# Kernel optimization log

Measured on AMD Instinct MI355X. Metric: run time of the kernel, lower is better.

The kernel has to match this reference:

```python
import jax, jax.numpy as jnp
import numpy as np
from jax import lax

N, CIN, H, W = 32, 128, 64, 64
COUT, KH, KW = 256, 3, 3
STRIDE = (1, 1)
PADDING = ((1, 1), (1, 1))


def setup_inputs() -> dict:
    key = jax.random.key(0)
    k1, k2, k3, k4 = jax.random.split(key, 4)
    # binary input in {0,1}
    x = jax.random.randint(k1, (N, CIN, H, W), 0, 2).astype(jnp.float32)
    # ternary weight in {-1,0,1}
    weight = (jax.random.randint(k2, (COUT, CIN, KH, KW), 0, 3) - 1).astype(jnp.float32)
    # integer bias (folded from BN, floored to int per get_sign_bias_from_bn)
    bias = jax.random.randint(k3, (COUT,), -200, 200).astype(jnp.float32)
    # sign in {-1,+1}, broadcast shape (1, COUT, 1, 1)
    sign = jnp.where(jax.random.bernoulli(k4, 0.5, (1, COUT, 1, 1)), 1.0, -1.0).astype(jnp.float32)
    return {"x": x, "weight": weight, "bias": bias, "sign": sign}


def reference(x, weight, bias, sign):
    # y = conv2d(x, W) + bias  (stride 1, pad 1, NCHW)
    y = lax.conv_general_dilated(
        x, weight,
        window_strides=STRIDE,
        padding=PADDING,
        dimension_numbers=("NCHW", "OIHW", "NCHW"),
    ) + bias[None, :, None, None]
    # rounding=True -> torch.round_(y)
    y = jnp.round(y)
    # output = 1 iff sign * y >= 0, cast back to input dtype
    return jnp.where(y * sign >= 0, jnp.float32(1), jnp.float32(0)).astype(x.dtype)
```

## Files before the change

kernel.cpp:

```cpp
#include <hip/hip_runtime.h>
#include <cstdint>


#define NIMG 32
#define CIN  128
#define HH   64
#define WW   64
#define COUT 256
#define PH   66
#define XT_ROWSTRIDE (PH * CIN)
#define XT_NSTRIDE   (PH * PH * CIN)
#define XT_BYTES     ((size_t)NIMG * XT_NSTRIDE)
#define WP_TAPSTRIDE (COUT * CIN)
#define WP_BYTES     ((size_t)9 * WP_TAPSTRIDE)

typedef int   v4i  __attribute__((ext_vector_type(4)));
typedef int   v16i __attribute__((ext_vector_type(16)));

__global__ __launch_bounds__(256) void xt_prepass(const float* __restrict__ x,
                                                  int8_t* __restrict__ xt) {
    const int py = blockIdx.x;
    const int n  = blockIdx.y;
    const int t  = threadIdx.x;
    int8_t* rowbase = xt + (size_t)(n * PH + py) * XT_ROWSTRIDE;

    if (py == 0 || py == PH - 1) {
        int4 z = {0, 0, 0, 0};
        for (int j = t; j < XT_ROWSTRIDE / 16; j += 256)
            ((int4*)rowbase)[j] = z;
        return;
    }

    __shared__ __align__(16) int8_t Ls[64 * 144];
    const int y  = py - 1;
    const int xq = t & 15;
    const float4* xf = (const float4*)x;
#pragma unroll
    for (int j = 0; j < 8; ++j) {
        const int ci = (t >> 4) + j * 16;
        float4 v = xf[((size_t)(n * CIN + ci) * HH + y) * 16 + xq];
        const int xv = xq * 4;
        Ls[(xv + 0) * 144 + ci] = (int8_t)v.x;
        Ls[(xv + 1) * 144 + ci] = (int8_t)v.y;
        Ls[(xv + 2) * 144 + ci] = (int8_t)v.z;
        Ls[(xv + 3) * 144 + ci] = (int8_t)v.w;
    }
    __syncthreads();
    const int4 z = {0, 0, 0, 0};
    for (int j = t; j < XT_ROWSTRIDE / 16; j += 256) {
        const int px  = j >> 3;
        const int c   = j & 7;
        int4 val;
        if (px == 0 || px == PH - 1) val = z;
        else                         val = *(const int4*)&Ls[(px - 1) * 144 + c * 16];
        *(int4*)(rowbase + (size_t)px * CIN + ((c ^ (px & 7)) << 4)) = val;
    }
}

__global__ __launch_bounds__(256) void w_prepack(const float* __restrict__ w,
                                                 int8_t* __restrict__ wq) {
    const int idx = blockIdx.x * 256 + threadIdx.x;
    if (idx >= (int)WP_BYTES) return;
    const int tap = idx >> 15;
    const int rem = idx & 32767;
    const int co  = rem >> 7;
    const int ci  = rem & 127;
    const int s = ci >> 5, hi = (ci >> 4) & 1, b = ci & 15;
    const int co32 = co >> 5, lo = co & 31;
    wq[(((tap * 8 + co32) * 4 + s) << 10) + ((hi * 32 + lo) << 4) + b] =
        (int8_t)w[(size_t)(co * CIN + ci) * 9 + tap];
}

__device__ __forceinline__ void glds16(const void* g, uint32_t lds_off) {
    asm volatile("s_mov_b32 m0, %0\n"
                 "global_load_lds_dwordx4 %1, off"
                 :: "s"(lds_off), "v"(g) : "memory");
}

__global__ __launch_bounds__(256) void binconv_gemm(
    const int8_t* __restrict__ xt, const int8_t* __restrict__ wq,
    const float* __restrict__ bias, const float* __restrict__ sign,
    float* __restrict__ out) {

    __shared__ __align__(16) int8_t Xraw[4 * XT_ROWSTRIDE];

    const int t    = threadIdx.x;
    const int wid  = t >> 6;
    const int lane = t & 63;
    const int bx   = blockIdx.x;
    const int co0  = blockIdx.y * 128;
    const int n    = bx >> 5;
    const int y0   = (bx & 31) << 1;

    const int8_t* xbase = xt + (size_t)n * XT_NSTRIDE + (size_t)y0 * XT_ROWSTRIDE;
    {
        const int8_t* gsrc = xbase + lane * 16;
        const uint32_t lds0 = (uint32_t)(uintptr_t)Xraw;
        for (int j = wid; j < 33; j += 4)
            glds16(gsrc + j * 1024,
                   __builtin_amdgcn_readfirstlane(lds0 + j * 1024));
        asm volatile("s_waitcnt vmcnt(0)" ::: "memory");
        __syncthreads();
    }

    const int m_lo = lane & 31;
    const int hi   = lane >> 5;
    const int co_off = (wid >> 1) * 64;
    const int yw     = wid & 1;
    const int ct0  = (co0 + co_off) >> 5;

    const int8_t* Xw  = Xraw + yw * XT_ROWSTRIDE;
    const int8_t* wqb = wq + lane * 16;

    v16i acc[2][2] = {};

#pragma unroll
    for (int tap = 0; tap < 9; ++tap) {
        const int ky = tap / 3, kx = tap % 3;
        const int8_t* xl = Xw + ky * XT_ROWSTRIDE;
        const int px0 = m_lo + kx;
        const int pk  = px0 & 7;

        v4i af[2][4];
#pragma unroll
        for (int c = 0; c < 2; ++c)
#pragma unroll
            for (int s = 0; s < 4; ++s)
                af[c][s] = *(const v4i*)(wqb
                    + ((((tap * 8 + ct0 + c) * 4) + s) << 10));

        const int8_t* xb = xl + px0 * CIN;
        v4i bf[2][4];
#pragma unroll
        for (int s = 0; s < 4; ++s) {
            const int sw = ((2 * s + hi) ^ pk) << 4;
#pragma unroll
            for (int m = 0; m < 2; ++m)
                bf[m][s] = *(const v4i*)(xb + m * 32 * CIN + sw);
        }
#pragma unroll
        for (int s = 0; s < 4; ++s)
#pragma unroll
            for (int c = 0; c < 2; ++c)
#pragma unroll
                for (int m = 0; m < 2; ++m)
                    acc[c][m] = __builtin_amdgcn_mfma_i32_32x32x32_i8(
                        af[c][s], bf[m][s], acc[c][m], 0, 0, 0);
    }

    const float* bco = bias + co0 + co_off;
    const float* sco = sign + co0 + co_off;
    float* outb = out + ((size_t)n * COUT + co0 + co_off) * (HH * WW)
                + (y0 + yw) * WW;
#pragma unroll
    for (int c = 0; c < 2; ++c) {
#pragma unroll
        for (int r = 0; r < 16; ++r) {
            const int co_l = c * 32 + (r & 3) + 8 * (r >> 2) + 4 * hi;
            const int bi = (int)bco[co_l];
            const int si = (int)sco[co_l];
            float* orow = outb + (size_t)co_l * (HH * WW);
#pragma unroll
            for (int m = 0; m < 2; ++m) {
                const int tv = (acc[c][m][r] + bi) * si;
                orow[m * 32 + m_lo] = (tv >= 0) ? 1.0f : 0.0f;
            }
        }
    }
}

__global__ __launch_bounds__(256) void naive_conv(
    const float* __restrict__ x, const float* __restrict__ w,
    const float* __restrict__ bias, const float* __restrict__ sign,
    float* __restrict__ out) {
    const int idx = blockIdx.x * 256 + threadIdx.x;
    const int xc = idx & 63, y = (idx >> 6) & 63, co = (idx >> 12) & 255,
              n = idx >> 20;
    float s = 0.f;
    for (int ci = 0; ci < CIN; ++ci)
        for (int ky = 0; ky < 3; ++ky) {
            const int iy = y + ky - 1;
            if (iy < 0 || iy >= HH) continue;
            for (int kx = 0; kx < 3; ++kx) {
                const int ix = xc + kx - 1;
                if (ix < 0 || ix >= WW) continue;
                s += x[((size_t)(n * CIN + ci) * HH + iy) * WW + ix] *
                     w[((size_t)(co * CIN + ci) * 3 + ky) * 3 + kx];
            }
        }
    const float yv = s + bias[co];
    out[idx] = ((sign[co] > 0.f) ? (yv >= 0.f) : (yv <= 0.f)) ? 1.0f : 0.0f;
}

extern "C" void kernel_launch(void* const* d_in, const int* in_sizes, int n_in,
                              void* d_out, int out_size, void* d_ws, size_t ws_size,
                              hipStream_t stream) {
    const float* x    = (const float*)d_in[0];
    const float* w    = (const float*)d_in[1];
    const float* bias = (const float*)d_in[2];
    const float* sign = (const float*)d_in[3];
    float* out = (float*)d_out;

    const size_t need = XT_BYTES + WP_BYTES;
    if (ws_size < need) {
        naive_conv<<<dim3((NIMG * COUT * HH * WW) / 256), 256, 0, stream>>>(
            x, w, bias, sign, out);
        return;
    }
    int8_t* xt = (int8_t*)d_ws;
    int8_t* wq = (int8_t*)d_ws + XT_BYTES;

    xt_prepass<<<dim3(PH, NIMG), 256, 0, stream>>>(x, xt);
    w_prepack<<<dim3((int)(WP_BYTES + 255) / 256), 256, 0, stream>>>(w, wq);
    binconv_gemm<<<dim3(NIMG * (HH / 2), COUT / 128), 256, 0, stream>>>(
        xt, wq, bias, sign, out);
}
```

Baseline: 228.3 us.

## Switch binary conv GEMM to FP4 scaled MFMA with LDS-staged vectorized output

Activations and ternary weights are now packed into 4-bit FP4 (E2M1) codes, two per byte. The GEMM uses the scaled f8f6f4 MFMA (32x32x64) with unit scales in place of int8 32x32x32, which halves the K steps and the bytes staged into LDS. The epilogue writes thresholded bits to LDS first, then emits coalesced 16-byte nontemporal float4 stores instead of scattered scalar stores. The price is bit-packing work in the prepass and reliance on FP4 encoding being exact for values in {-1,0,1}, plus fp32 accumulation staying exact for integer sums.

```diff
diff --git a/kernel.cpp b/kernel.cpp
--- a/kernel.cpp
+++ b/kernel.cpp
@@ -8,25 +8,32 @@
 #define WW   64
 #define COUT 256
 #define PH   66
-#define XT_ROWSTRIDE (PH * CIN)
-#define XT_NSTRIDE   (PH * PH * CIN)
-#define XT_BYTES     ((size_t)NIMG * XT_NSTRIDE)
-#define WP_TAPSTRIDE (COUT * CIN)
-#define WP_BYTES     ((size_t)9 * WP_TAPSTRIDE)
+#define X4_ROW 4224
+#define X4_IMG (PH * X4_ROW)
+#define X4_BYTES ((size_t)NIMG * X4_IMG)
+#define WQ4_BYTES ((size_t)9 * 8 * 2 * 64 * 16)
 
 typedef int   v4i  __attribute__((ext_vector_type(4)));
-typedef int   v16i __attribute__((ext_vector_type(16)));
+typedef int   v8i  __attribute__((ext_vector_type(8)));
+typedef float v16f __attribute__((ext_vector_type(16)));
+typedef float v4f  __attribute__((ext_vector_type(4)));
+
+__device__ __forceinline__ uint32_t pack4(uint32_t u) {
+    const uint32_t tt = (u & 0x01010101u) << 1;
+    return (tt & 0xFu) | ((tt >> 4) & 0xF0u) | ((tt >> 8) & 0xF00u)
+         | ((tt >> 12) & 0xF000u);
+}
 
 __global__ __launch_bounds__(256) void xt_prepass(const float* __restrict__ x,
-                                                  int8_t* __restrict__ xt) {
+                                                  int8_t* __restrict__ xt4) {
     const int py = blockIdx.x;
     const int n  = blockIdx.y;
     const int t  = threadIdx.x;
-    int8_t* rowbase = xt + (size_t)(n * PH + py) * XT_ROWSTRIDE;
+    int8_t* rowbase = xt4 + (size_t)(n * PH + py) * X4_ROW;
 
     if (py == 0 || py == PH - 1) {
         int4 z = {0, 0, 0, 0};
-        for (int j = t; j < XT_ROWSTRIDE / 16; j += 256)
+        for (int j = t; j < X4_ROW / 16; j += 256)
             ((int4*)rowbase)[j] = z;
         return;
     }
@@ -46,29 +53,38 @@
         Ls[(xv + 3) * 144 + ci] = (int8_t)v.w;
     }
     __syncthreads();
-    const int4 z = {0, 0, 0, 0};
-    for (int j = t; j < XT_ROWSTRIDE / 16; j += 256) {
-        const int px  = j >> 3;
-        const int c   = j & 7;
-        int4 val;
-        if (px == 0 || px == PH - 1) val = z;
-        else                         val = *(const int4*)&Ls[(px - 1) * 144 + c * 16];
-        *(int4*)(rowbase + (size_t)px * CIN + ((c ^ (px & 7)) << 4)) = val;
+    for (int j = t; j < 264; j += 256) {
+        const int px = j >> 2;
+        const int c  = j & 3;
+        int4 o = {0, 0, 0, 0};
+        if (px != 0 && px != PH - 1) {
+            const int4* lp = (const int4*)&Ls[(px - 1) * 144 + c * 32];
+            const int4 a = lp[0], b = lp[1];
+            o.x = (int)(pack4((uint32_t)a.x) | (pack4((uint32_t)a.y) << 16));
+            o.y = (int)(pack4((uint32_t)a.z) | (pack4((uint32_t)a.w) << 16));
+            o.z = (int)(pack4((uint32_t)b.x) | (pack4((uint32_t)b.y) << 16));
+            o.w = (int)(pack4((uint32_t)b.z) | (pack4((uint32_t)b.w) << 16));
+        }
+        *(int4*)(rowbase + (size_t)px * 64 + ((c ^ (px & 3)) << 4)) = o;
     }
 }
 
 __global__ __launch_bounds__(256) void w_prepack(const float* __restrict__ w,
-                                                 int8_t* __restrict__ wq) {
+                                                 int8_t* __restrict__ wq4) {
     const int idx = blockIdx.x * 256 + threadIdx.x;
-    if (idx >= (int)WP_BYTES) return;
-    const int tap = idx >> 15;
-    const int rem = idx & 32767;
-    const int co  = rem >> 7;
-    const int ci  = rem & 127;
-    const int s = ci >> 5, hi = (ci >> 4) & 1, b = ci & 15;
-    const int co32 = co >> 5, lo = co & 31;
-    wq[(((tap * 8 + co32) * 4 + s) << 10) + ((hi * 32 + lo) << 4) + b] =
-        (int8_t)w[(size_t)(co * CIN + ci) * 9 + tap];
+    if (idx >= (int)WQ4_BYTES) return;
+    const int b    = idx & 15;
+    const int lane = (idx >> 4) & 63;
+    const int s    = (idx >> 10) & 1;
+    const int co32 = (idx >> 11) & 7;
+    const int tap  = idx >> 14;
+    const int co   = co32 * 32 + (lane & 31);
+    const int ci0  = s * 64 + (lane >> 5) * 32 + b * 2;
+    const int i0 = (int)w[(size_t)(co * CIN + ci0) * 9 + tap];
+    const int i1 = (int)w[(size_t)(co * CIN + ci0 + 1) * 9 + tap];
+    const uint32_t n0 = (i0 == 0) ? 0u : ((i0 > 0) ? 0x2u : 0xAu);
+    const uint32_t n1 = (i1 == 0) ? 0u : ((i1 > 0) ? 0x2u : 0xAu);
+    wq4[idx] = (int8_t)(n0 | (n1 << 4));
 }
 
 __device__ __forceinline__ void glds16(const void* g, uint32_t lds_off) {
@@ -77,12 +93,17 @@
                  :: "s"(lds_off), "v"(g) : "memory");
 }
 
+__device__ __forceinline__ v8i widen(v4i x) {
+    v8i r = {x[0], x[1], x[2], x[3], 0, 0, 0, 0};
+    return r;
+}
+
 __global__ __launch_bounds__(256) void binconv_gemm(
-    const int8_t* __restrict__ xt, const int8_t* __restrict__ wq,
+    const int8_t* __restrict__ xt4, const int8_t* __restrict__ wq4,
     const float* __restrict__ bias, const float* __restrict__ sign,
     float* __restrict__ out) {
 
-    __shared__ __align__(16) int8_t Xraw[4 * XT_ROWSTRIDE];
+    __shared__ __align__(16) int8_t Xraw[17 * 1024];
 
     const int t    = threadIdx.x;
     const int wid  = t >> 6;
@@ -92,11 +113,11 @@
     const int n    = bx >> 5;
     const int y0   = (bx & 31) << 1;
 
-    const int8_t* xbase = xt + (size_t)n * XT_NSTRIDE + (size_t)y0 * XT_ROWSTRIDE;
+    const int8_t* xbase = xt4 + (size_t)n * X4_IMG + (size_t)y0 * X4_ROW;
     {
         const int8_t* gsrc = xbase + lane * 16;
         const uint32_t lds0 = (uint32_t)(uintptr_t)Xraw;
-        for (int j = wid; j < 33; j += 4)
+        for (int j = wid; j < 17; j += 4)
             glds16(gsrc + j * 1024,
                    __builtin_amdgcn_readfirstlane(lds0 + j * 1024));
         asm volatile("s_waitcnt vmcnt(0)" ::: "memory");
@@ -107,65 +128,83 @@
     const int hi   = lane >> 5;
     const int co_off = (wid >> 1) * 64;
     const int yw     = wid & 1;
-    const int ct0  = (co0 + co_off) >> 5;
-
-    const int8_t* Xw  = Xraw + yw * XT_ROWSTRIDE;
-    const int8_t* wqb = wq + lane * 16;
-
-    v16i acc[2][2] = {};
+    const int ct0    = (co0 + co_off) >> 5;
+
+    const int8_t* Xw   = Xraw + yw * X4_ROW;
+    const int8_t* wqb  = wq4 + lane * 16;
+
+    v16f acc[2][2] = {};
 
 #pragma unroll
     for (int tap = 0; tap < 9; ++tap) {
         const int ky = tap / 3, kx = tap % 3;
-        const int8_t* xl = Xw + ky * XT_ROWSTRIDE;
+        const int8_t* xl = Xw + ky * X4_ROW;
         const int px0 = m_lo + kx;
-        const int pk  = px0 & 7;
-
-        v4i af[2][4];
+        const int pk  = px0 & 3;
+
+        v4i af[2][2];
 #pragma unroll
         for (int c = 0; c < 2; ++c)
 #pragma unroll
-            for (int s = 0; s < 4; ++s)
+            for (int s = 0; s < 2; ++s)
                 af[c][s] = *(const v4i*)(wqb
-                    + ((((tap * 8 + ct0 + c) * 4) + s) << 10));
-
-        const int8_t* xb = xl + px0 * CIN;
-        v4i bf[2][4];
-#pragma unroll
-        for (int s = 0; s < 4; ++s) {
-            const int sw = ((2 * s + hi) ^ pk) << 4;
+                    + ((((tap * 8 + ct0 + c) * 2) + s) << 10));
+
+        v4i bf[2][2];
+#pragma unroll
+        for (int s = 0; s < 2; ++s) {
+            const int sw = (((s << 1) + hi) ^ pk) << 4;
 #pragma unroll
             for (int m = 0; m < 2; ++m)
-                bf[m][s] = *(const v4i*)(xb + m * 32 * CIN + sw);
-        }
-#pragma unroll
-        for (int s = 0; s < 4; ++s)
+                bf[m][s] = *(const v4i*)(xl + (px0 + m * 32) * 64 + sw);
+        }
+#pragma unroll
+        for (int s = 0; s < 2; ++s)
 #pragma unroll
             for (int c = 0; c < 2; ++c)
 #pragma unroll
                 for (int m = 0; m < 2; ++m)
-                    acc[c][m] = __builtin_amdgcn_mfma_i32_32x32x32_i8(
-                        af[c][s], bf[m][s], acc[c][m], 0, 0, 0);
-    }
+                    acc[c][m] = __builtin_amdgcn_mfma_scale_f32_32x32x64_f8f6f4(
+                        widen(af[c][s]), widen(bf[m][s]), acc[c][m],
+                        4, 4,
+                        0, 0x7F7F7F7F,
+                        0, 0x7F7F7F7F);
+    }
+
+    __syncthreads();
+    int8_t* Lep = Xraw + wid * 4096;
 
     const float* bco = bias + co0 + co_off;
     const float* sco = sign + co0 + co_off;
+#pragma unroll
+    for (int c = 0; c < 2; ++c) {
+#pragma unroll
+        for (int r = 0; r < 16; ++r) {
+            const int co_l = c * 32 + (r & 3) + 8 * (r >> 2) + 4 * hi;
+            const float bv = bco[co_l];
+            const float sv = sco[co_l];
+#pragma unroll
+            for (int m = 0; m < 2; ++m) {
+                const float yv = acc[c][m][r] + bv;
+                const bool on = (sv > 0.0f) ? (yv >= 0.0f) : (yv <= 0.0f);
+                Lep[co_l * 64 + m * 32 + m_lo] = (int8_t)on;
+            }
+        }
+    }
+    const int r16 = lane & 15, q4 = lane >> 4;
     float* outb = out + ((size_t)n * COUT + co0 + co_off) * (HH * WW)
                 + (y0 + yw) * WW;
 #pragma unroll
-    for (int c = 0; c < 2; ++c) {
-#pragma unroll
-        for (int r = 0; r < 16; ++r) {
-            const int co_l = c * 32 + (r & 3) + 8 * (r >> 2) + 4 * hi;
-            const int bi = (int)bco[co_l];
-            const int si = (int)sco[co_l];
-            float* orow = outb + (size_t)co_l * (HH * WW);
-#pragma unroll
-            for (int m = 0; m < 2; ++m) {
-                const int tv = (acc[c][m][r] + bi) * si;
-                orow[m * 32 + m_lo] = (tv >= 0) ? 1.0f : 0.0f;
-            }
-        }
+    for (int g = 0; g < 16; ++g) {
+        const int p = g * 4 + q4;
+        const uint32_t u = *(const uint32_t*)&Lep[p * 64 + r16 * 4];
+        v4f v;
+        v.x = (float)( u        & 0xff);
+        v.y = (float)((u >>  8) & 0xff);
+        v.z = (float)((u >> 16) & 0xff);
+        v.w = (float)((u >> 24) & 0xff);
+        __builtin_nontemporal_store(v,
+            (v4f*)(outb + (size_t)p * (HH * WW) + r16 * 4));
     }
 }
 
@@ -201,17 +240,17 @@
     const float* sign = (const float*)d_in[3];
     float* out = (float*)d_out;
 
-    const size_t need = XT_BYTES + WP_BYTES;
+    const size_t need = X4_BYTES + WQ4_BYTES + 1024;
     if (ws_size < need) {
         naive_conv<<<dim3((NIMG * COUT * HH * WW) / 256), 256, 0, stream>>>(
             x, w, bias, sign, out);
         return;
     }
-    int8_t* xt = (int8_t*)d_ws;
-    int8_t* wq = (int8_t*)d_ws + XT_BYTES;
-
-    xt_prepass<<<dim3(PH, NIMG), 256, 0, stream>>>(x, xt);
-    w_prepack<<<dim3((int)(WP_BYTES + 255) / 256), 256, 0, stream>>>(w, wq);
+    int8_t* xt4 = (int8_t*)d_ws;
+    int8_t* wq4 = (int8_t*)d_ws + X4_BYTES;
+
+    xt_prepass<<<dim3(PH, NIMG), 256, 0, stream>>>(x, xt4);
+    w_prepack<<<dim3((int)((WQ4_BYTES + 255) / 256)), 256, 0, stream>>>(w, wq4);
     binconv_gemm<<<dim3(NIMG * (HH / 2), COUT / 128), 256, 0, stream>>>(
-        xt, wq, bias, sign, out);
-}
+        xt4, wq4, bias, sign, out);
+}
```

Measured after the change: 209.3 us. -8.3%, faster.
